# Kernel optimization log

Measured on AMD Instinct MI355X. Metric: run time of the kernel, lower is better.

The kernel has to match this reference:

```python
import jax, jax.numpy as jnp
import numpy as np

N_NODES = 100000
N_EDGES = 3200000
N_GRAPHS = 512
HID = 64
OUT = 10


def setup_inputs() -> dict:
    key = jax.random.key(0)
    ks = jax.random.split(key, 10)
    x = jax.random.normal(ks[0], (N_NODES,), dtype=jnp.float32)
    edge_index = jax.random.randint(ks[1], (2, N_EDGES), 0, N_NODES, dtype=jnp.int64)
    batch = jnp.sort(jax.random.randint(ks[2], (N_NODES,), 0, N_GRAPHS, dtype=jnp.int64))
    # GCNConv weights (glorot) and zero biases, Linear layer params
    W1 = jax.random.normal(ks[3], (1, HID), dtype=jnp.float32) * (1.0 / np.sqrt(1 + HID))
    b1 = jnp.zeros((HID,), dtype=jnp.float32)
    W2 = jax.random.normal(ks[4], (HID, HID), dtype=jnp.float32) * (1.0 / np.sqrt(2 * HID))
    b2 = jnp.zeros((HID,), dtype=jnp.float32)
    Wl = jax.random.normal(ks[5], (2 * HID, OUT), dtype=jnp.float32) * (1.0 / np.sqrt(2 * HID))
    bl = jnp.zeros((OUT,), dtype=jnp.float32)
    return {"x": x, "edge_index": edge_index, "batch": batch,
            "W1": W1, "b1": b1, "W2": W2, "b2": b2, "Wl": Wl, "bl": bl}


def reference(x, edge_index, batch, W1, b1, W2, b2, Wl, bl):
    N = x.shape[0]
    loop = jnp.arange(N, dtype=edge_index.dtype)
    src = jnp.concatenate([edge_index[0], loop])  # add self-loops
    dst = jnp.concatenate([edge_index[1], loop])
    # symmetric GCN normalization: D^{-1/2} A_hat D^{-1/2}
    deg = jax.ops.segment_sum(jnp.ones_like(dst, dtype=jnp.float32), dst, num_segments=N)
    dinv = jax.lax.rsqrt(jnp.maximum(deg, 1.0))
    norm = (dinv[src] * dinv[dst])[:, None]  # [E+N, 1]

    def gcn(h, W, b):
        m = (h @ W)[src] * norm  # transform then gather messages
        return jax.ops.segment_sum(m, dst, num_segments=N) + b

    h0 = x[:, None]  # [N, 1] (dropout is identity at eval)
    x1 = jax.nn.relu(gcn(h0, W1, b1))
    x2 = jax.nn.relu(gcn(x1, W2, b2))
    xj = jnp.concatenate([x1, x2], axis=-1)  # JK 'cat' -> [N, 128]
    # global mean pool per graph
    cnt = jax.ops.segment_sum(jnp.ones((N,), jnp.float32), batch, num_segments=N_GRAPHS)
    pooled = jax.ops.segment_sum(xj, batch, num_segments=N_GRAPHS) / jnp.maximum(cnt, 1.0)[:, None]
    return pooled @ Wl + bl  # [G, 10]
```

## Files before the change

### kernel.cpp

```cpp
#include <hip/hip_runtime.h>
#include <hip/hip_bf16.h>

#define N_NODES 100000
#define N_EDGES 3200000
#define N_GRAPHS 512
#define HID 64
#define OUT_DIM 10

#define NPB 64
#define NB  1563
#define CAP 2432

__global__ __launch_bounds__(256) void k_part(const int4* __restrict__ src4,
                                              const int4* __restrict__ dst4,
                                              unsigned* __restrict__ bcur,
                                              unsigned* __restrict__ ebuf) {
    __shared__ unsigned hist[NB];
    int tid = threadIdx.x;
    for (int i = tid; i < NB; i += 256) hist[i] = 0;
    __syncthreads();
    int base4 = (blockIdx.x * 256 + tid) * 2;
    int4 s0 = make_int4(-1, -1, -1, -1), s1 = s0;
    int4 d0 = make_int4(0, 0, 0, 0), d1 = d0;
    if (base4 < N_EDGES / 4)     { s0 = src4[base4];     d0 = dst4[base4]; }
    if (base4 + 1 < N_EDGES / 4) { s1 = src4[base4 + 1]; d1 = dst4[base4 + 1]; }
    int sv[8] = { s0.x, s0.y, s0.z, s0.w, s1.x, s1.y, s1.z, s1.w };
    int dv[8] = { d0.x, d0.y, d0.z, d0.w, d1.x, d1.y, d1.z, d1.w };
    int bk[8]; unsigned rk[8];
    #pragma unroll
    for (int k = 0; k < 8; k++) {
        bk[k] = dv[k] >> 6;
        rk[k] = (sv[k] >= 0) ? atomicAdd(&hist[bk[k]], 1u) : 0u;
    }
    __syncthreads();
    for (int i = tid; i < NB; i += 256) {
        unsigned c = hist[i];
        hist[i] = c ? atomicAdd(&bcur[i], c) : 0u;
    }
    __syncthreads();
    #pragma unroll
    for (int k = 0; k < 8; k++) {
        if (sv[k] >= 0) {
            unsigned dl = (unsigned)(dv[k] & 63);
            ebuf[(size_t)bk[k] * CAP + hist[bk[k]] + rk[k]] = (dl << 24) | (unsigned)sv[k];
        }
    }
}

__global__ __launch_bounds__(256) void k_buck1(const unsigned* __restrict__ ebuf,
                                               const unsigned* __restrict__ bcur,
                                               const float* __restrict__ x,
                                               unsigned* __restrict__ deg,
                                               float* __restrict__ dinv,
                                               float* __restrict__ g1,
                                               unsigned* __restrict__ ebuf2) {
    __shared__ unsigned cnt[NPB];
    __shared__ int offs[NPB];
    __shared__ unsigned rnk[CAP];
    int b = blockIdx.x, tid = threadIdx.x;
    if (tid < NPB) cnt[tid] = 0;
    __syncthreads();
    int ec = (int)bcur[b];
    const unsigned* eb = ebuf + (size_t)b * CAP;
    unsigned* eb2 = ebuf2 + (size_t)b * CAP;
    for (int i = tid; i < ec; i += 256)
        rnk[i] = atomicAdd(&cnt[eb[i] >> 24], 1u);
    __syncthreads();
    if (tid == 0) {
        int r = 0;
        for (int i = 0; i < NPB; i++) { offs[i] = r; r += (int)cnt[i]; }
    }
    __syncthreads();
    int n0 = b * NPB;
    int nn = min(NPB, N_NODES - n0);
    if (tid < nn) {
        unsigned c = cnt[tid];
        float dn = 1.0f / sqrtf((float)c + 1.0f);
        deg[n0 + tid] = c;
        dinv[n0 + tid] = dn;
        g1[n0 + tid] = dn * x[n0 + tid];
    }
    for (int i = tid; i < ec; i += 256) {
        unsigned w = eb[i];
        eb2[offs[w >> 24] + rnk[i]] = w;
    }
}

__global__ __launch_bounds__(256) void k_buck2(const unsigned* __restrict__ ebuf2,
                                               const unsigned* __restrict__ bcur,
                                               const float* __restrict__ g1,
                                               const float* __restrict__ dinv,
                                               const float* __restrict__ x,
                                               float2* __restrict__ sd) {
    __shared__ float sacc[NPB];
    int b = blockIdx.x, tid = threadIdx.x;
    if (tid < NPB) sacc[tid] = 0.f;
    __syncthreads();
    int ec = (int)bcur[b];
    const unsigned* eb = ebuf2 + (size_t)b * CAP;
    for (int i = tid; i < ec; i += 256) {
        unsigned w = eb[i];
        atomicAdd(&sacc[w >> 24], g1[w & 0x00FFFFFFu]);
    }
    __syncthreads();
    int n0 = b * NPB;
    int nn = min(NPB, N_NODES - n0);
    if (tid < nn) {
        float dn = dinv[n0 + tid];
        float s = dn * (sacc[tid] + dn * x[n0 + tid]);
        sd[n0 + tid] = make_float2(s, dn);
    }
}

__global__ __launch_bounds__(256) void k_buck3(const unsigned* __restrict__ ebuf2,
                                               const unsigned* __restrict__ bcur,
                                               const unsigned* __restrict__ deg,
                                               const float2* __restrict__ sd,
                                               const int* __restrict__ batch,
                                               const float* __restrict__ W1,
                                               const float* __restrict__ b1,
                                               const float* __restrict__ W2,
                                               const float* __restrict__ b2,
                                               float* __restrict__ pooled) {
    __shared__ float w2ls[HID * HID];
    __shared__ float2 stage[256];
    __shared__ int offs[NPB + 1];
    int b = blockIdx.x, tid = threadIdx.x;
    int lane = tid & 63, wv = tid >> 6;
    int n0 = b * NPB;
    int nn = min(NPB, N_NODES - n0);
    if (tid == 0) {
        int r = 0;
        for (int i = 0; i < nn; i++) { offs[i] = r; r += (int)deg[n0 + i]; }
        offs[nn] = r;
    }
    for (int i = tid; i < HID * HID; i += 256) w2ls[i] = W2[i];
    float w1 = W1[lane], bb1 = b1[lane], bb2 = b2[lane];
    __syncthreads();
    const unsigned* eb2 = ebuf2 + (size_t)b * CAP;
    float2* st = stage + wv * 64;
    const float4* stv = (const float4*)st;
    int curg = -1;
    float pacc1 = 0.f, pacc2 = 0.f;

    auto fetchv = [&](int n) -> float2 {
        float2 v = make_float2(0.f, 0.f);
        if (n < nn) {
            int lo = offs[n];
            int m = offs[n + 1] - lo; if (m > 64) m = 64;
            if (lane < m) v = sd[eb2[lo + lane] & 0x00FFFFFFu];
        }
        return v;
    };

    float2 vcur = fetchv(wv);
    for (int n = wv; n < nn; n += 4) {
        float2 vnext = fetchv(n + 4);
        int lo = offs[n], hi = offs[n + 1];
        int m = hi - lo; if (m > 64) m = 64;
        st[lane] = vcur;
        float acca = 0.f, accb = 0.f;
        int k = 0;
        for (; k + 1 < m; k += 2) {
            float4 e = stv[k >> 1];
            acca = fmaf(e.y, fmaxf(fmaf(e.x, w1, bb1), 0.f), acca);
            accb = fmaf(e.w, fmaxf(fmaf(e.z, w1, bb1), 0.f), accb);
        }
        if (k < m) {
            float2 e0 = st[k];
            acca = fmaf(e0.y, fmaxf(fmaf(e0.x, w1, bb1), 0.f), acca);
        }
        for (int base = lo + 64; base < hi; base += 64) {
            int mm = hi - base; if (mm > 64) mm = 64;
            float2 v = make_float2(0.f, 0.f);
            if (lane < mm) v = sd[eb2[base + lane] & 0x00FFFFFFu];
            st[lane] = v;
            int kk = 0;
            for (; kk + 1 < mm; kk += 2) {
                float4 e = stv[kk >> 1];
                acca = fmaf(e.y, fmaxf(fmaf(e.x, w1, bb1), 0.f), acca);
                accb = fmaf(e.w, fmaxf(fmaf(e.z, w1, bb1), 0.f), accb);
            }
            if (kk < mm) {
                float2 e0 = st[kk];
                acca = fmaf(e0.y, fmaxf(fmaf(e0.x, w1, bb1), 0.f), acca);
            }
        }
        float2 self = sd[n0 + n];
        float t = fmaxf(fmaf(self.x, w1, bb1), 0.f);
        float a = self.y * (acca + accb + self.y * t);
        float acc2a = bb2, acc2b = 0.f;
        #pragma unroll
        for (int j = 0; j < HID; j += 2) {
            float aj0 = __int_as_float(__builtin_amdgcn_readlane(__float_as_int(a), j));
            float aj1 = __int_as_float(__builtin_amdgcn_readlane(__float_as_int(a), j + 1));
            acc2a = fmaf(aj0, w2ls[j * HID + lane], acc2a);
            acc2b = fmaf(aj1, w2ls[(j + 1) * HID + lane], acc2b);
        }
        float x2v = fmaxf(acc2a + acc2b, 0.f);
        int g = batch[n0 + n];
        if (g != curg) {
            if (curg >= 0) {
                atomicAdd(&pooled[curg * 2 * HID + lane], pacc1);
                atomicAdd(&pooled[curg * 2 * HID + HID + lane], pacc2);
            }
            curg = g; pacc1 = 0.f; pacc2 = 0.f;
        }
        pacc1 += t;
        pacc2 += x2v;
        vcur = vnext;
    }
    if (curg >= 0) {
        atomicAdd(&pooled[curg * 2 * HID + lane], pacc1);
        atomicAdd(&pooled[curg * 2 * HID + HID + lane], pacc2);
    }
}

__global__ __launch_bounds__(128) void k_head(const float* __restrict__ pooled,
                                              const int* __restrict__ batch,
                                              const float* __restrict__ Wl,
                                              const float* __restrict__ bl,
                                              float* __restrict__ out) {
    int g = blockIdx.x;
    int t = threadIdx.x;
    int lo1 = 0, hi1 = N_NODES;
    while (lo1 < hi1) { int mid = (lo1 + hi1) >> 1; if (batch[mid] < g) lo1 = mid + 1; else hi1 = mid; }
    int lo2 = lo1, hi2 = N_NODES;
    while (lo2 < hi2) { int mid = (lo2 + hi2) >> 1; if (batch[mid] < g + 1) lo2 = mid + 1; else hi2 = mid; }
    float denom = fmaxf((float)(lo2 - lo1), 1.f);
    __shared__ float pl[2 * HID];
    pl[t] = pooled[g * 2 * HID + t] / denom;
    __syncthreads();
    if (t < OUT_DIM) {
        float r = bl[t];
        #pragma unroll 16
        for (int j = 0; j < 2 * HID; j++) r = fmaf(pl[j], Wl[j * OUT_DIM + t], r);
        out[g * OUT_DIM + t] = r;
    }
}

extern "C" void kernel_launch(void* const* d_in, const int* in_sizes, int n_in,
                              void* d_out, int out_size, void* d_ws, size_t ws_size,
                              hipStream_t stream) {
    const float* x      = (const float*)d_in[0];
    const int*   ei     = (const int*)d_in[1];
    const int*   batch  = (const int*)d_in[2];
    const float* W1     = (const float*)d_in[3];
    const float* b1     = (const float*)d_in[4];
    const float* W2     = (const float*)d_in[5];
    const float* b2     = (const float*)d_in[6];
    const float* Wl     = (const float*)d_in[7];
    const float* bl     = (const float*)d_in[8];
    float* out = (float*)d_out;

    const int* src = ei;
    const int* dst = ei + N_EDGES;

    char* p = (char*)d_ws;
    auto alloc = [&](size_t bytes) { void* r = (void*)p; p += (bytes + 255) & ~(size_t)255; return r; };
    unsigned* bcur   = (unsigned*)alloc(NB * 4);
    unsigned* ebuf   = (unsigned*)alloc((size_t)NB * CAP * 4);
    unsigned* ebuf2  = (unsigned*)alloc((size_t)NB * CAP * 4);
    unsigned* deg    = (unsigned*)alloc(N_NODES * 4);
    float*    dinv   = (float*)alloc(N_NODES * 4);
    float*    g1     = (float*)alloc(N_NODES * 4);
    float2*   sd     = (float2*)alloc((size_t)N_NODES * 8);
    float*    pooled = (float*)alloc((size_t)N_GRAPHS * 2 * HID * 4);

    hipMemsetAsync(bcur, 0, NB * 4, stream);
    hipMemsetAsync(pooled, 0, (size_t)N_GRAPHS * 2 * HID * 4, stream);

    const int TB = 256;
    int pbl = (N_EDGES / 8 + TB - 1) / TB;

    k_part <<<pbl, TB, 0, stream>>>((const int4*)src, (const int4*)dst, bcur, ebuf);
    k_buck1<<<NB, TB, 0, stream>>>(ebuf, bcur, x, deg, dinv, g1, ebuf2);
    k_buck2<<<NB, TB, 0, stream>>>(ebuf2, bcur, g1, dinv, x, sd);
    k_buck3<<<NB, TB, 0, stream>>>(ebuf2, bcur, deg, sd, batch, W1, b1, W2, b2, pooled);
    k_head <<<N_GRAPHS, 128, 0, stream>>>(pooled, batch, Wl, bl, out);
}
```

Before: 291.3 us.

## Drop second edge buffer; pack rank into edge word and scatter-gather in LDS

Instead of a second sorted edge buffer, k_buck1 writes each edge's within-node rank into the upper bits of the existing packed word, which now uses a 17-bit source field. k_buck3 computes padded per-node offsets with a wave scan, then scatters the gathered sd values for the whole bucket into a large LDS stage, ordered by node. Per-node accumulation then reads contiguously from LDS. This removes the ebuf2 global write and read round-trip and the serial offset loop, at the cost of roughly 20KB of extra LDS per block, which may lower occupancy. It also removes the overlapped prefetch of the next node's neighbours.

```diff
diff --git a/kernel.cpp b/kernel.cpp
--- a/kernel.cpp
+++ b/kernel.cpp
@@ -10,6 +10,8 @@
 #define NPB 64
 #define NB  1563
 #define CAP 2432
+#define CAP2 (CAP + NPB)
+
 
 __global__ __launch_bounds__(256) void k_part(const int4* __restrict__ src4,
                                               const int4* __restrict__ dst4,
@@ -42,33 +44,27 @@
     for (int k = 0; k < 8; k++) {
         if (sv[k] >= 0) {
             unsigned dl = (unsigned)(dv[k] & 63);
-            ebuf[(size_t)bk[k] * CAP + hist[bk[k]] + rk[k]] = (dl << 24) | (unsigned)sv[k];
-        }
-    }
-}
-
-__global__ __launch_bounds__(256) void k_buck1(const unsigned* __restrict__ ebuf,
+            ebuf[(size_t)bk[k] * CAP + hist[bk[k]] + rk[k]] = (dl << 17) | (unsigned)sv[k];
+        }
+    }
+}
+
+__global__ __launch_bounds__(256) void k_buck1(unsigned* __restrict__ ebuf,
                                                const unsigned* __restrict__ bcur,
                                                const float* __restrict__ x,
                                                unsigned* __restrict__ deg,
                                                float* __restrict__ dinv,
-                                               float* __restrict__ g1,
-                                               unsigned* __restrict__ ebuf2) {
+                                               float* __restrict__ g1) {
     __shared__ unsigned cnt[NPB];
-    __shared__ int offs[NPB];
-    __shared__ unsigned rnk[CAP];
     int b = blockIdx.x, tid = threadIdx.x;
     if (tid < NPB) cnt[tid] = 0;
     __syncthreads();
     int ec = (int)bcur[b];
-    const unsigned* eb = ebuf + (size_t)b * CAP;
-    unsigned* eb2 = ebuf2 + (size_t)b * CAP;
-    for (int i = tid; i < ec; i += 256)
-        rnk[i] = atomicAdd(&cnt[eb[i] >> 24], 1u);
-    __syncthreads();
-    if (tid == 0) {
-        int r = 0;
-        for (int i = 0; i < NPB; i++) { offs[i] = r; r += (int)cnt[i]; }
+    unsigned* eb = ebuf + (size_t)b * CAP;
+    for (int i = tid; i < ec; i += 256) {
+        unsigned w = eb[i];
+        unsigned rk = atomicAdd(&cnt[(w >> 17) & 63], 1u);
+        eb[i] = w | (rk << 23);
     }
     __syncthreads();
     int n0 = b * NPB;
@@ -80,13 +76,9 @@
         dinv[n0 + tid] = dn;
         g1[n0 + tid] = dn * x[n0 + tid];
     }
-    for (int i = tid; i < ec; i += 256) {
-        unsigned w = eb[i];
-        eb2[offs[w >> 24] + rnk[i]] = w;
-    }
-}
-
-__global__ __launch_bounds__(256) void k_buck2(const unsigned* __restrict__ ebuf2,
+}
+
+__global__ __launch_bounds__(256) void k_buck2(const unsigned* __restrict__ ebuf,
                                                const unsigned* __restrict__ bcur,
                                                const float* __restrict__ g1,
                                                const float* __restrict__ dinv,
@@ -97,10 +89,10 @@
     if (tid < NPB) sacc[tid] = 0.f;
     __syncthreads();
     int ec = (int)bcur[b];
-    const unsigned* eb = ebuf2 + (size_t)b * CAP;
+    const unsigned* eb = ebuf + (size_t)b * CAP;
     for (int i = tid; i < ec; i += 256) {
         unsigned w = eb[i];
-        atomicAdd(&sacc[w >> 24], g1[w & 0x00FFFFFFu]);
+        atomicAdd(&sacc[(w >> 17) & 63], g1[w & 0x1FFFFu]);
     }
     __syncthreads();
     int n0 = b * NPB;
@@ -112,7 +104,7 @@
     }
 }
 
-__global__ __launch_bounds__(256) void k_buck3(const unsigned* __restrict__ ebuf2,
+__global__ __launch_bounds__(256) void k_buck3(const unsigned* __restrict__ ebuf,
                                                const unsigned* __restrict__ bcur,
                                                const unsigned* __restrict__ deg,
                                                const float2* __restrict__ sd,
@@ -122,69 +114,55 @@
                                                const float* __restrict__ W2,
                                                const float* __restrict__ b2,
                                                float* __restrict__ pooled) {
+    __shared__ __align__(16) float2 stage2[CAP2];
     __shared__ float w2ls[HID * HID];
-    __shared__ float2 stage[256];
     __shared__ int offs[NPB + 1];
+    __shared__ int degs[NPB];
     int b = blockIdx.x, tid = threadIdx.x;
     int lane = tid & 63, wv = tid >> 6;
     int n0 = b * NPB;
     int nn = min(NPB, N_NODES - n0);
-    if (tid == 0) {
-        int r = 0;
-        for (int i = 0; i < nn; i++) { offs[i] = r; r += (int)deg[n0 + i]; }
-        offs[nn] = r;
-    }
     for (int i = tid; i < HID * HID; i += 256) w2ls[i] = W2[i];
+    if (wv == 0) {
+        int d = (lane < nn) ? (int)deg[n0 + lane] : 0;
+        degs[lane] = d;
+        int dp = (d + 1) & ~1;
+        int sum = dp;
+        #pragma unroll
+        for (int o = 1; o < 64; o <<= 1) {
+            int t = __shfl_up(sum, o, 64);
+            if (lane >= o) sum += t;
+        }
+        offs[lane + 1] = sum;
+        offs[lane]     = sum - dp;
+        if (lane == 0) offs[0] = 0;
+    }
     float w1 = W1[lane], bb1 = b1[lane], bb2 = b2[lane];
     __syncthreads();
-    const unsigned* eb2 = ebuf2 + (size_t)b * CAP;
-    float2* st = stage + wv * 64;
-    const float4* stv = (const float4*)st;
+    int ec = (int)bcur[b];
+    const unsigned* eb = ebuf + (size_t)b * CAP;
+    for (int i = tid; i < ec; i += 256) {
+        unsigned w = eb[i];
+        stage2[offs[(w >> 17) & 63] + (w >> 23)] = sd[w & 0x1FFFFu];
+    }
+    __syncthreads();
+    const float4* stv = (const float4*)stage2;
     int curg = -1;
     float pacc1 = 0.f, pacc2 = 0.f;
-
-    auto fetchv = [&](int n) -> float2 {
-        float2 v = make_float2(0.f, 0.f);
-        if (n < nn) {
-            int lo = offs[n];
-            int m = offs[n + 1] - lo; if (m > 64) m = 64;
-            if (lane < m) v = sd[eb2[lo + lane] & 0x00FFFFFFu];
-        }
-        return v;
-    };
-
-    float2 vcur = fetchv(wv);
     for (int n = wv; n < nn; n += 4) {
-        float2 vnext = fetchv(n + 4);
-        int lo = offs[n], hi = offs[n + 1];
-        int m = hi - lo; if (m > 64) m = 64;
-        st[lane] = vcur;
+        int lo = offs[n];
+        int m = degs[n];
         float acca = 0.f, accb = 0.f;
-        int k = 0;
-        for (; k + 1 < m; k += 2) {
-            float4 e = stv[k >> 1];
+        int half = m >> 1;
+        int p0 = lo >> 1;
+        for (int k = 0; k < half; k++) {
+            float4 e = stv[p0 + k];
             acca = fmaf(e.y, fmaxf(fmaf(e.x, w1, bb1), 0.f), acca);
             accb = fmaf(e.w, fmaxf(fmaf(e.z, w1, bb1), 0.f), accb);
         }
-        if (k < m) {
-            float2 e0 = st[k];
+        if (m & 1) {
+            float2 e0 = stage2[lo + m - 1];
             acca = fmaf(e0.y, fmaxf(fmaf(e0.x, w1, bb1), 0.f), acca);
-        }
-        for (int base = lo + 64; base < hi; base += 64) {
-            int mm = hi - base; if (mm > 64) mm = 64;
-            float2 v = make_float2(0.f, 0.f);
-            if (lane < mm) v = sd[eb2[base + lane] & 0x00FFFFFFu];
-            st[lane] = v;
-            int kk = 0;
-            for (; kk + 1 < mm; kk += 2) {
-                float4 e = stv[kk >> 1];
-                acca = fmaf(e.y, fmaxf(fmaf(e.x, w1, bb1), 0.f), acca);
-                accb = fmaf(e.w, fmaxf(fmaf(e.z, w1, bb1), 0.f), accb);
-            }
-            if (kk < mm) {
-                float2 e0 = st[kk];
-                acca = fmaf(e0.y, fmaxf(fmaf(e0.x, w1, bb1), 0.f), acca);
-            }
         }
         float2 self = sd[n0 + n];
         float t = fmaxf(fmaf(self.x, w1, bb1), 0.f);
@@ -208,7 +186,6 @@
         }
         pacc1 += t;
         pacc2 += x2v;
-        vcur = vnext;
     }
     if (curg >= 0) {
         atomicAdd(&pooled[curg * 2 * HID + lane], pacc1);
@@ -260,7 +237,6 @@
     auto alloc = [&](size_t bytes) { void* r = (void*)p; p += (bytes + 255) & ~(size_t)255; return r; };
     unsigned* bcur   = (unsigned*)alloc(NB * 4);
     unsigned* ebuf   = (unsigned*)alloc((size_t)NB * CAP * 4);
-    unsigned* ebuf2  = (unsigned*)alloc((size_t)NB * CAP * 4);
     unsigned* deg    = (unsigned*)alloc(N_NODES * 4);
     float*    dinv   = (float*)alloc(N_NODES * 4);
     float*    g1     = (float*)alloc(N_NODES * 4);
@@ -274,8 +250,8 @@
     int pbl = (N_EDGES / 8 + TB - 1) / TB;
 
     k_part <<<pbl, TB, 0, stream>>>((const int4*)src, (const int4*)dst, bcur, ebuf);
-    k_buck1<<<NB, TB, 0, stream>>>(ebuf, bcur, x, deg, dinv, g1, ebuf2);
-    k_buck2<<<NB, TB, 0, stream>>>(ebuf2, bcur, g1, dinv, x, sd);
-    k_buck3<<<NB, TB, 0, stream>>>(ebuf2, bcur, deg, sd, batch, W1, b1, W2, b2, pooled);
+    k_buck1<<<NB, TB, 0, stream>>>(ebuf, bcur, x, deg, dinv, g1);
+    k_buck2<<<NB, TB, 0, stream>>>(ebuf, bcur, g1, dinv, x, sd);
+    k_buck3<<<NB, TB, 0, stream>>>(ebuf, bcur, deg, sd, batch, W1, b1, W2, b2, pooled);
     k_head <<<N_GRAPHS, 128, 0, stream>>>(pooled, batch, Wl, bl, out);
 }
```

Measured after the change: 266.9 us. -8.4%, faster.
